# Kernel optimization log

Measured on AMD Instinct MI355X. Metric: run time of the kernel, lower is better.

Reference implementation:

```python
import jax, jax.numpy as jnp
import numpy as np

D_MODEL = 2048
N_HEADS = 16
HEAD_DIM = D_MODEL // N_HEADS  # 128
B, S = 4, 2048


def setup_inputs() -> dict:
    key = jax.random.key(0)
    ks = jax.random.split(key, 7)
    scale = 1.0 / np.sqrt(D_MODEL)
    return {
        "x": jax.random.normal(ks[0], (B, S, D_MODEL), dtype=jnp.float32),
        "cos": jax.random.uniform(ks[1], (S, HEAD_DIM // 2), dtype=jnp.float32),
        "sin": jax.random.uniform(ks[2], (S, HEAD_DIM // 2), dtype=jnp.float32),
        "Wq": jax.random.normal(ks[3], (D_MODEL, D_MODEL), dtype=jnp.float32) * scale,
        "Wk": jax.random.normal(ks[4], (D_MODEL, D_MODEL), dtype=jnp.float32) * scale,
        "Wv": jax.random.normal(ks[5], (D_MODEL, D_MODEL), dtype=jnp.float32) * scale,
        "Wo": jax.random.normal(ks[6], (D_MODEL, D_MODEL), dtype=jnp.float32) * scale,
    }


def apply_rope(x, cos, sin):
    # x: [B, H, S, head_dim]; cos/sin: [S, half] (split-in-half RoPE)
    half = x.shape[-1] // 2
    x1, x2 = x[..., :half], x[..., half:]
    cos = cos[None, None, :, :].astype(x.dtype)
    sin = sin[None, None, :, :].astype(x.dtype)
    return jnp.concatenate([x1 * cos - x2 * sin, x1 * sin + x2 * cos], axis=-1)


def reference(x, cos, sin, Wq, Wk, Wv, Wo):
    Bx, Sx, _ = x.shape
    # nn.Linear: y = x @ W.T
    def proj(W):
        y = jnp.einsum("bsd,ed->bse", x, W)
        return y.reshape(Bx, Sx, N_HEADS, HEAD_DIM).transpose(0, 2, 1, 3)  # [B,H,S,hd]
    q = apply_rope(proj(Wq), cos, sin)
    k = apply_rope(proj(Wk), cos, sin)
    v = proj(Wv)
    scale = 1.0 / np.sqrt(HEAD_DIM)
    scores = jnp.einsum("bhqd,bhkd->bhqk", q, k) * scale  # [B,H,S,S]
    attn = jax.nn.softmax(scores, axis=-1)
    out = jnp.einsum("bhqk,bhkd->bhqd", attn, v)
    out = out.transpose(0, 2, 1, 3).reshape(Bx, Sx, D_MODEL)
    return jnp.einsum("bsd,ed->bse", out, Wo)
```

## Files before the change

### kernel.cpp

```cpp
#include <hip/hip_runtime.h>

typedef _Float16 half_t;
typedef __attribute__((ext_vector_type(8))) _Float16 half8;
typedef __attribute__((ext_vector_type(4))) _Float16 half4v;
typedef __attribute__((ext_vector_type(4))) float f32x4;

#define MFMA16(a,b,c) __builtin_amdgcn_mfma_f32_16x16x32_f16((a),(b),(c),0,0,0)

__device__ __forceinline__ void gld_lds16(const half_t* g, half_t* l){
    __builtin_amdgcn_global_load_lds((__attribute__((address_space(1))) void*)(g),
                                     (__attribute__((address_space(3))) void*)(l), 16, 0, 0);
}

__global__ __launch_bounds__(256) void cvt_k(const float* __restrict__ s, half_t* __restrict__ d, int n4){
    int i = blockIdx.x * 256 + threadIdx.x;
    if (i < n4){
        float4 v = ((const float4*)s)[i];
        half4v h = { (half_t)v.x, (half_t)v.y, (half_t)v.z, (half_t)v.w };
        ((half4v*)d)[i] = h;
    }
}

__global__ __launch_bounds__(256) void cvtw_k(const float* __restrict__ w0, const float* __restrict__ w1,
                                              const float* __restrict__ w2, const float* __restrict__ w3,
                                              half_t* __restrict__ dst){
    const float* srcs[4] = {w0, w1, w2, w3};
    const float* s = srcs[blockIdx.y];
    int i = blockIdx.x * 256 + threadIdx.x;
    float4 v = ((const float4*)s)[i];
    half4v h = { (half_t)v.x, (half_t)v.y, (half_t)v.z, (half_t)v.w };
    ((half4v*)(dst))[(size_t)blockIdx.y * 1048576 + i] = h;
}

__global__ __launch_bounds__(256) void gemm_nt(const half_t* __restrict__ A, const half_t* __restrict__ B,
                                               half_t* __restrict__ Qw, half_t* __restrict__ Kw,
                                               half_t* __restrict__ Vt, float* __restrict__ Co, int kind){
    const int tid  = threadIdx.x;
    const int lane = tid & 63;
    const int w    = lane >> 4;
    const int l15  = lane & 15;
    const int l7   = lane & 7;
    const int wav  = tid >> 6;
    const int wm   = (wav >> 1) * 64;
    const int wn   = (wav & 1) * 64;
    const int bm   = blockIdx.x;
    const int bn   = blockIdx.y;
    const int KD   = 2048;

    __shared__ __align__(16) half_t smem[16384];
    half_t* As = smem;
    half_t* Bs = smem + 8192;

    f32x4 acc[4][4] = {};

    const half_t* Ab = A + (size_t)bm * 128 * KD;
    const half_t* Bb = B + (size_t)bn * 128 * KD;

    for (int k0 = 0; k0 < KD; k0 += 64){
#pragma unroll
        for (int i = 0; i < 4; i++){
            int c = tid + i*256;
            int r = c >> 3, p = c & 7;
            gld_lds16(Ab + (size_t)r*KD + k0 + ((p ^ (r&7)) << 3), As + c*8);
        }
#pragma unroll
        for (int i = 0; i < 4; i++){
            int c = tid + i*256;
            int r = c >> 3, p = c & 7;
            gld_lds16(Bb + (size_t)r*KD + k0 + ((p ^ (r&7)) << 3), Bs + c*8);
        }
        __syncthreads();
#pragma unroll
        for (int ks = 0; ks < 2; ks++){
            half8 af[4], bf[4];
#pragma unroll
            for (int mi = 0; mi < 4; mi++)
                af[mi] = *(const half8*)(As + (wm + mi*16 + l15)*64 + (((ks*4 + w) ^ l7) << 3));
#pragma unroll
            for (int ni = 0; ni < 4; ni++)
                bf[ni] = *(const half8*)(Bs + (wn + ni*16 + l15)*64 + (((ks*4 + w) ^ l7) << 3));
#pragma unroll
            for (int mi = 0; mi < 4; mi++)
#pragma unroll
                for (int ni = 0; ni < 4; ni++)
                    acc[mi][ni] = MFMA16(af[mi], bf[ni], acc[mi][ni]);
        }
        __syncthreads();
    }

    const int rbase = wm + w*4;
    const int cbase = wn + l15;

    if (kind == 0){
        const int which = bn >> 4;
        const int nb = (bn & 15) * 128;
        if (which < 2){
            half_t* dst = which ? Kw : Qw;
#pragma unroll
            for (int mi = 0; mi < 4; mi++)
#pragma unroll
                for (int ni = 0; ni < 4; ni++)
#pragma unroll
                    for (int r = 0; r < 4; r++){
                        int m = bm*128 + rbase + mi*16 + r;
                        int n = nb + cbase + ni*16;
                        dst[(((size_t)(m>>11)*16 + (n>>7))*2048 + (m&2047))*128 + (n&127)] = (half_t)acc[mi][ni][r];
                    }
        } else {
#pragma unroll
            for (int mi = 0; mi < 4; mi++)
#pragma unroll
                for (int ni = 0; ni < 4; ni++){
                    int m0 = bm*128 + rbase + mi*16;
                    int n  = nb + cbase + ni*16;
                    half4v h = {(half_t)acc[mi][ni][0], (half_t)acc[mi][ni][1],
                                (half_t)acc[mi][ni][2], (half_t)acc[mi][ni][3]};
                    *(half4v*)(Vt + (((size_t)(m0>>11)*16 + (n>>7))*128 + (n&127))*2048 + (m0&2047)) = h;
                }
        }
    } else {
#pragma unroll
        for (int mi = 0; mi < 4; mi++)
#pragma unroll
            for (int ni = 0; ni < 4; ni++)
#pragma unroll
                for (int r = 0; r < 4; r++){
                    int m = bm*128 + rbase + mi*16 + r;
                    int n = bn*128 + cbase + ni*16;
                    Co[(size_t)m*2048 + n] = acc[mi][ni][r];
                }
    }
}

__global__ __launch_bounds__(256) void rope_k(half_t* __restrict__ Qw, half_t* __restrict__ Kw,
                                              const float* __restrict__ cs, const float* __restrict__ sn){
    int t  = blockIdx.x * 256 + threadIdx.x;
    int d  = t & 63;
    int s  = (t >> 6) & 2047;
    int bh = t >> 17;
    float c  = cs[s*64 + d];
    float si = sn[s*64 + d];
    size_t base = ((size_t)bh*2048 + s)*128 + d;
    float q1 = (float)Qw[base], q2 = (float)Qw[base+64];
    Qw[base]    = (half_t)(q1*c - q2*si);
    Qw[base+64] = (half_t)(q1*si + q2*c);
    float k1 = (float)Kw[base], k2 = (float)Kw[base+64];
    Kw[base]    = (half_t)(k1*c - k2*si);
    Kw[base+64] = (half_t)(k1*si + k2*c);
}

__global__ __launch_bounds__(256, 3) void attn_k(const half_t* __restrict__ Q, const half_t* __restrict__ K,
                                                 const half_t* __restrict__ Vt, half_t* __restrict__ AO){
    const int tid  = threadIdx.x;
    const int lane = tid & 63;
    const int w    = lane >> 4;
    const int l15  = lane & 15;
    const int l7   = lane & 7;
    const int wav  = tid >> 6;
    const int qt   = blockIdx.x;
    const int bh   = blockIdx.y;

    __shared__ __align__(16) half_t smem[8192 + 8192 + 4*2304];
    half_t* Ks = smem;
    half_t* Vs = smem + 8192;
    half_t* Ps = smem + 16384 + wav*2304;
    half_t* Ob = smem + wav*4096;

    const half_t* Qb = Q + ((size_t)bh*2048 + qt*128 + wav*32)*128;
    half8 aq[2][4];
#pragma unroll
    for (int qi = 0; qi < 2; qi++)
#pragma unroll
        for (int ks = 0; ks < 4; ks++)
            aq[qi][ks] = *(const half8*)(Qb + (qi*16 + l15)*128 + ks*32 + w*8);

    f32x4 oacc[8][2] = {};
    float m_[2] = {-1e30f, -1e30f};
    float l_[2] = {0.0f, 0.0f};

    const float SSC = 0.08838834764831845f * 1.4426950408889634f;

    for (int kt = 0; kt < 32; kt++){
        const half_t* Kb = K  + ((size_t)bh*2048 + kt*64)*128;
        const half_t* Vb = Vt + (size_t)bh*128*2048 + kt*64;
        __syncthreads();
#pragma unroll
        for (int i = 0; i < 4; i++){
            int c = tid + i*256;
            int key = c >> 4, pc = c & 15;
            gld_lds16(Kb + key*128 + ((pc ^ (key&7)) << 3), Ks + c*8);
        }
#pragma unroll
        for (int i = 0; i < 4; i++){
            int c = tid + i*256;
            int d = c >> 3, pc = c & 7;
            gld_lds16(Vb + (size_t)d*2048 + ((pc ^ (d&7)) << 3), Vs + c*8);
        }
        __syncthreads();

        f32x4 sacc[4][2] = {};
#pragma unroll
        for (int ks = 0; ks < 4; ks++){
#pragma unroll
            for (int t = 0; t < 4; t++){
                half8 kf = *(const half8*)(Ks + (t*16 + l15)*128 + (((ks*4 + w) ^ l7) << 3));
                sacc[t][0] = MFMA16(kf, aq[0][ks], sacc[t][0]);
                sacc[t][1] = MFMA16(kf, aq[1][ks], sacc[t][1]);
            }
        }

#pragma unroll
        for (int qi = 0; qi < 2; qi++){
            float mx = sacc[0][qi][0];
#pragma unroll
            for (int t = 0; t < 4; t++)
#pragma unroll
                for (int r = 0; r < 4; r++) mx = fmaxf(mx, sacc[t][qi][r]);
            mx = fmaxf(mx, __shfl_xor(mx, 16));
            mx = fmaxf(mx, __shfl_xor(mx, 32));
            float mn = fmaxf(m_[qi], mx*SSC);
            float alpha = exp2f(m_[qi] - mn);
            m_[qi] = mn;
            float sum = 0.0f;
#pragma unroll
            for (int t = 0; t < 4; t++){
                float p0 = exp2f(sacc[t][qi][0]*SSC - mn);
                float p1 = exp2f(sacc[t][qi][1]*SSC - mn);
                float p2 = exp2f(sacc[t][qi][2]*SSC - mn);
                float p3 = exp2f(sacc[t][qi][3]*SSC - mn);
                sum += (p0 + p1) + (p2 + p3);
                half4v hv = {(half_t)p0, (half_t)p1, (half_t)p2, (half_t)p3};
                *(half4v*)(Ps + (qi*16 + l15)*72 + t*16 + w*4) = hv;
            }
            sum += __shfl_xor(sum, 16);
            sum += __shfl_xor(sum, 32);
            l_[qi] = l_[qi]*alpha + sum;
#pragma unroll
            for (int t = 0; t < 8; t++)
#pragma unroll
                for (int r = 0; r < 4; r++) oacc[t][qi][r] *= alpha;
        }

#pragma unroll
        for (int c2 = 0; c2 < 2; c2++){
            half8 pf0 = *(const half8*)(Ps + l15*72        + c2*32 + w*8);
            half8 pf1 = *(const half8*)(Ps + (16 + l15)*72 + c2*32 + w*8);
#pragma unroll
            for (int t = 0; t < 8; t++){
                half8 vf = *(const half8*)(Vs + (t*16 + l15)*64 + (((c2*4 + w) ^ l7) << 3));
                oacc[t][0] = MFMA16(vf, pf0, oacc[t][0]);
                oacc[t][1] = MFMA16(vf, pf1, oacc[t][1]);
            }
        }
    }

    float inv[2] = {1.0f / l_[0], 1.0f / l_[1]};
    __syncthreads();
#pragma unroll
    for (int t = 0; t < 8; t++)
#pragma unroll
        for (int qi = 0; qi < 2; qi++){
            int q  = qi*16 + l15;
            int c8 = t*2 + (w>>1);
            int pc = c8 ^ l7;
            half4v hv = {(half_t)(oacc[t][qi][0]*inv[qi]), (half_t)(oacc[t][qi][1]*inv[qi]),
                         (half_t)(oacc[t][qi][2]*inv[qi]), (half_t)(oacc[t][qi][3]*inv[qi])};
            *(half4v*)(Ob + q*128 + pc*8 + (w&1)*4) = hv;
        }
    const int b = bh >> 4, h = bh & 15;
#pragma unroll
    for (int it = 0; it < 8; it++){
        int q  = it*4 + w;
        half8 rd = *(const half8*)(Ob + q*128 + ((l15 ^ (q&7)) << 3));
        int s = qt*128 + wav*32 + q;
        *(half8*)(AO + ((size_t)(b*2048 + s))*2048 + h*128 + l15*8) = rd;
    }
}

extern "C" void kernel_launch(void* const* d_in, const int* in_sizes, int n_in,
                              void* d_out, int out_size, void* d_ws, size_t ws_size,
                              hipStream_t stream){
    const float* x  = (const float*)d_in[0];
    const float* cs = (const float*)d_in[1];
    const float* sn = (const float*)d_in[2];
    const float* Wq = (const float*)d_in[3];
    const float* Wk = (const float*)d_in[4];
    const float* Wv = (const float*)d_in[5];
    const float* Wo = (const float*)d_in[6];

    half_t* ws = (half_t*)d_ws;
    half_t* xh = ws;
    half_t* w4 = ws + (size_t)16777216;
    half_t* qw = ws + (size_t)33554432;
    half_t* kw = ws + (size_t)50331648;
    half_t* vt = ws + (size_t)67108864;
    half_t* ao = ws + (size_t)83886080;

    cvt_k<<<16384, 256, 0, stream>>>(x, xh, 4194304);
    cvtw_k<<<dim3(4096, 4), 256, 0, stream>>>(Wq, Wk, Wv, Wo, w4);

    gemm_nt<<<dim3(64, 48), 256, 0, stream>>>(xh, w4, qw, kw, vt, nullptr, 0);
    rope_k<<<32768, 256, 0, stream>>>(qw, kw, cs, sn);
    attn_k<<<dim3(16, 64), 256, 0, stream>>>(qw, kw, vt, ao);
    gemm_nt<<<dim3(64, 16), 256, 0, stream>>>(ao, w4 + 12582912, nullptr, nullptr, nullptr,
                                              (float*)d_out, 1);
}
```

Measured before the change: 786.7 us.

## Replace GEMM with 256x256 multi-stage pipelined kernel and skip redundant softmax rescale

The 128x128 single-buffered GEMM becomes a 512-thread, 256x256-tile kernel. It uses a multi-stage LDS pipeline with direct global-to-LDS loads, explicit vmcnt waits, barriers, MFMA priority boosts and a swizzled workgroup order for L2 reuse. The goal is to hide load latency and raise MFMA utilisation in the QKV and output projections. Separately, the attention softmax now skips the alpha rescale of the accumulators when no lane's running max increases. Risks are fewer workgroups per CU from the 128KB LDS footprint and fragile hand-scheduled wait counts.

```diff
diff --git a/kernel.cpp b/kernel.cpp
--- a/kernel.cpp
+++ b/kernel.cpp
@@ -32,103 +32,121 @@
     ((half4v*)(dst))[(size_t)blockIdx.y * 1048576 + i] = h;
 }
 
-__global__ __launch_bounds__(256) void gemm_nt(const half_t* __restrict__ A, const half_t* __restrict__ B,
-                                               half_t* __restrict__ Qw, half_t* __restrict__ Kw,
-                                               half_t* __restrict__ Vt, float* __restrict__ Co, int kind){
+#define VMWAIT_(n) asm volatile("s_waitcnt vmcnt(" #n ")" ::: "memory")
+#define VMWAIT(n)  VMWAIT_(n)
+
+#define STAGE8(hh) { \
+    const int Tt2 = (hh) >> 2, jj2 = (hh) & 3; \
+    half_t* db = smem + ((jj2 & 1) << 15) + ((Tt2 & 1) << 14) + ((jj2 >> 1) << 13); \
+    const half_t* Gs = ((jj2 & 1) ? Bg : Ag) + Tt2*64 + ((jj2 >> 1) << 5); \
+    gld_lds16(Gs + off0, db + d0); \
+    gld_lds16(Gs + off1, db + d1); \
+}
+
+#define PHASE8(Tt, jj, hh, VMN) { \
+    half_t* Ah = smem + (((Tt) & 1) << 14) + (((jj) >> 1) << 13); \
+    half_t* Bh = Ah + 32768; \
+    half8 af[4], bf[4]; \
+    _Pragma("unroll") for (int x = 0; x < 4; x++) af[x] = *(const half8*)(Ah + (((jj)&1)*4 + x)*1024 + cA); \
+    _Pragma("unroll") for (int y = 0; y < 4; y++) bf[y] = *(const half8*)(Bh + y*1024 + cB); \
+    if ((hh) < 128) STAGE8(hh); \
+    if ((jj) & 1) VMWAIT(VMN); \
+    asm volatile("s_barrier" ::: "memory"); \
+    __builtin_amdgcn_s_setprio(1); \
+    _Pragma("unroll") for (int x = 0; x < 4; x++) \
+      _Pragma("unroll") for (int y = 0; y < 4; y++) \
+        acc[((jj)&1)*4 + x][y] = MFMA16(af[x], bf[y], acc[((jj)&1)*4 + x][y]); \
+    __builtin_amdgcn_s_setprio(0); \
+    __builtin_amdgcn_sched_barrier(0); \
+    asm volatile("s_barrier" ::: "memory"); \
+}
+
+__global__ __launch_bounds__(512) void gemm8(const half_t* __restrict__ A, const half_t* __restrict__ B,
+                                             half_t* __restrict__ Qw, half_t* __restrict__ Kw,
+                                             half_t* __restrict__ Vt, float* __restrict__ Co, int kind){
     const int tid  = threadIdx.x;
     const int lane = tid & 63;
-    const int w    = lane >> 4;
+    const int w4   = lane >> 4;
     const int l15  = lane & 15;
     const int l7   = lane & 7;
     const int wav  = tid >> 6;
-    const int wm   = (wav >> 1) * 64;
-    const int wn   = (wav & 1) * 64;
-    const int bm   = blockIdx.x;
-    const int bn   = blockIdx.y;
-    const int KD   = 2048;
-
-    __shared__ __align__(16) half_t smem[16384];
-    half_t* As = smem;
-    half_t* Bs = smem + 8192;
-
-    f32x4 acc[4][4] = {};
-
-    const half_t* Ab = A + (size_t)bm * 128 * KD;
-    const half_t* Bb = B + (size_t)bn * 128 * KD;
-
-    for (int k0 = 0; k0 < KD; k0 += 64){
-#pragma unroll
-        for (int i = 0; i < 4; i++){
-            int c = tid + i*256;
-            int r = c >> 3, p = c & 7;
-            gld_lds16(Ab + (size_t)r*KD + k0 + ((p ^ (r&7)) << 3), As + c*8);
-        }
-#pragma unroll
-        for (int i = 0; i < 4; i++){
-            int c = tid + i*256;
-            int r = c >> 3, p = c & 7;
-            gld_lds16(Bb + (size_t)r*KD + k0 + ((p ^ (r&7)) << 3), Bs + c*8);
-        }
-        __syncthreads();
-#pragma unroll
-        for (int ks = 0; ks < 2; ks++){
-            half8 af[4], bf[4];
-#pragma unroll
-            for (int mi = 0; mi < 4; mi++)
-                af[mi] = *(const half8*)(As + (wm + mi*16 + l15)*64 + (((ks*4 + w) ^ l7) << 3));
-#pragma unroll
-            for (int ni = 0; ni < 4; ni++)
-                bf[ni] = *(const half8*)(Bs + (wn + ni*16 + l15)*64 + (((ks*4 + w) ^ l7) << 3));
-#pragma unroll
-            for (int mi = 0; mi < 4; mi++)
-#pragma unroll
-                for (int ni = 0; ni < 4; ni++)
-                    acc[mi][ni] = MFMA16(af[mi], bf[ni], acc[mi][ni]);
-        }
-        __syncthreads();
-    }
-
-    const int rbase = wm + w*4;
-    const int cbase = wn + l15;
+    const int wavM = wav >> 2;
+    const int wnq  = wav & 3;
+
+    const int nwg = gridDim.x;
+    const int wg  = blockIdx.x;
+    const int swz = (wg & 7) * (nwg >> 3) + (wg >> 3);
+    const int bm  = swz & 31;
+    const int bn  = swz >> 5;
+
+    __shared__ __align__(16) half_t smem[65536];
+
+    const half_t* Ag = A + (size_t)bm * 256 * 2048;
+    const half_t* Bg = B + (size_t)bn * 256 * 2048;
+
+    const int p0  = tid >> 3, q0 = tid & 7, c0 = q0 ^ (p0 & 7);
+    const int off0 = (p0 + ((c0 >> 2) << 7)) * 2048 + ((c0 & 3) << 3);
+    const int off1 = off0 + 131072;
+    const int d0  = tid * 8, d1 = d0 + 4096;
+
+    const int cA = l15*64 + (((w4 | (wavM << 2)) ^ l7) << 3);
+    const int cB = ((wnq & 1)*64 + l15)*64 + (((w4 | ((wnq >> 1) << 2)) ^ l7) << 3);
+
+    f32x4 acc[8][4] = {};
+
+#pragma unroll
+    for (int h = 0; h < 6; h++) STAGE8(h);
+    VMWAIT(4);
+    asm volatile("s_barrier" ::: "memory");
+
+    for (int it = 0; it < 15; it++){
+        const int h0 = it*8 + 6;
+        PHASE8(2*it,   0, h0,     6); PHASE8(2*it,   1, h0 + 1, 6);
+        PHASE8(2*it,   2, h0 + 2, 6); PHASE8(2*it,   3, h0 + 3, 6);
+        PHASE8(2*it+1, 0, h0 + 4, 6); PHASE8(2*it+1, 1, h0 + 5, 6);
+        PHASE8(2*it+1, 2, h0 + 6, 6); PHASE8(2*it+1, 3, h0 + 7, 6);
+    }
+    PHASE8(30, 0, 126, 6); PHASE8(30, 1, 127, 6);
+    PHASE8(30, 2, 128, 6); PHASE8(30, 3, 129, 2);
+    PHASE8(31, 0, 130, 0); PHASE8(31, 1, 131, 0);
+    PHASE8(31, 2, 132, 0); PHASE8(31, 3, 133, 0);
+
+    const int mB = bm*256 + wavM*128 + w4*4;
+    const int nB = bn*256 + wnq*64 + l15;
 
     if (kind == 0){
-        const int which = bn >> 4;
-        const int nb = (bn & 15) * 128;
-        if (which < 2){
-            half_t* dst = which ? Kw : Qw;
-#pragma unroll
-            for (int mi = 0; mi < 4; mi++)
-#pragma unroll
-                for (int ni = 0; ni < 4; ni++)
+#pragma unroll
+        for (int mi = 0; mi < 8; mi++)
+#pragma unroll
+            for (int ni = 0; ni < 4; ni++){
+                int n  = nB + ni*16;
+                int which = n >> 11;
+                int nb = n & 2047;
+                int m0 = mB + mi*16;
+                if (which < 2){
+                    half_t* dst = which ? Kw : Qw;
 #pragma unroll
                     for (int r = 0; r < 4; r++){
-                        int m = bm*128 + rbase + mi*16 + r;
-                        int n = nb + cbase + ni*16;
-                        dst[(((size_t)(m>>11)*16 + (n>>7))*2048 + (m&2047))*128 + (n&127)] = (half_t)acc[mi][ni][r];
+                        int m = m0 + r;
+                        dst[(((size_t)(m >> 11)*16 + (nb >> 7))*2048 + (m & 2047))*128 + (nb & 127)] = (half_t)acc[mi][ni][r];
                     }
-        } else {
-#pragma unroll
-            for (int mi = 0; mi < 4; mi++)
-#pragma unroll
-                for (int ni = 0; ni < 4; ni++){
-                    int m0 = bm*128 + rbase + mi*16;
-                    int n  = nb + cbase + ni*16;
-                    half4v h = {(half_t)acc[mi][ni][0], (half_t)acc[mi][ni][1],
-                                (half_t)acc[mi][ni][2], (half_t)acc[mi][ni][3]};
-                    *(half4v*)(Vt + (((size_t)(m0>>11)*16 + (n>>7))*128 + (n&127))*2048 + (m0&2047)) = h;
+                } else {
+                    half4v hv = {(half_t)acc[mi][ni][0], (half_t)acc[mi][ni][1],
+                                 (half_t)acc[mi][ni][2], (half_t)acc[mi][ni][3]};
+                    *(half4v*)(Vt + (((size_t)(m0 >> 11)*16 + (nb >> 7))*128 + (nb & 127))*2048 + (m0 & 2047)) = hv;
                 }
-        }
+            }
     } else {
 #pragma unroll
-        for (int mi = 0; mi < 4; mi++)
-#pragma unroll
-            for (int ni = 0; ni < 4; ni++)
-#pragma unroll
-                for (int r = 0; r < 4; r++){
-                    int m = bm*128 + rbase + mi*16 + r;
-                    int n = bn*128 + cbase + ni*16;
-                    Co[(size_t)m*2048 + n] = acc[mi][ni][r];
-                }
+        for (int mi = 0; mi < 8; mi++)
+#pragma unroll
+            for (int ni = 0; ni < 4; ni++){
+                int n  = nB + ni*16;
+                int m0 = mB + mi*16;
+#pragma unroll
+                for (int r = 0; r < 4; r++)
+                    Co[(size_t)(m0 + r)*2048 + n] = acc[mi][ni][r];
+            }
     }
 }
 
@@ -218,27 +236,33 @@
                 for (int r = 0; r < 4; r++) mx = fmaxf(mx, sacc[t][qi][r]);
             mx = fmaxf(mx, __shfl_xor(mx, 16));
             mx = fmaxf(mx, __shfl_xor(mx, 32));
-            float mn = fmaxf(m_[qi], mx*SSC);
-            float alpha = exp2f(m_[qi] - mn);
-            m_[qi] = mn;
+            float mxs = mx * SSC;
+            unsigned long long upd = __ballot(mxs > m_[qi]);
+            if (upd){
+                float mn    = fmaxf(m_[qi], mxs);
+                float alpha = exp2f(m_[qi] - mn);
+                m_[qi] = mn;
+                l_[qi] *= alpha;
+#pragma unroll
+                for (int t = 0; t < 8; t++)
+#pragma unroll
+                    for (int r = 0; r < 4; r++) oacc[t][qi][r] *= alpha;
+            }
+            float mq = m_[qi];
             float sum = 0.0f;
 #pragma unroll
             for (int t = 0; t < 4; t++){
-                float p0 = exp2f(sacc[t][qi][0]*SSC - mn);
-                float p1 = exp2f(sacc[t][qi][1]*SSC - mn);
-                float p2 = exp2f(sacc[t][qi][2]*SSC - mn);
-                float p3 = exp2f(sacc[t][qi][3]*SSC - mn);
+                float p0 = exp2f(sacc[t][qi][0]*SSC - mq);
+                float p1 = exp2f(sacc[t][qi][1]*SSC - mq);
+                float p2 = exp2f(sacc[t][qi][2]*SSC - mq);
+                float p3 = exp2f(sacc[t][qi][3]*SSC - mq);
                 sum += (p0 + p1) + (p2 + p3);
                 half4v hv = {(half_t)p0, (half_t)p1, (half_t)p2, (half_t)p3};
                 *(half4v*)(Ps + (qi*16 + l15)*72 + t*16 + w*4) = hv;
             }
             sum += __shfl_xor(sum, 16);
             sum += __shfl_xor(sum, 32);
-            l_[qi] = l_[qi]*alpha + sum;
-#pragma unroll
-            for (int t = 0; t < 8; t++)
-#pragma unroll
-                for (int r = 0; r < 4; r++) oacc[t][qi][r] *= alpha;
+            l_[qi] += sum;
         }
 
 #pragma unroll
@@ -299,9 +323,9 @@
     cvt_k<<<16384, 256, 0, stream>>>(x, xh, 4194304);
     cvtw_k<<<dim3(4096, 4), 256, 0, stream>>>(Wq, Wk, Wv, Wo, w4);
 
-    gemm_nt<<<dim3(64, 48), 256, 0, stream>>>(xh, w4, qw, kw, vt, nullptr, 0);
+    gemm8<<<768, 512, 0, stream>>>(xh, w4, qw, kw, vt, nullptr, 0);
     rope_k<<<32768, 256, 0, stream>>>(qw, kw, cs, sn);
     attn_k<<<dim3(16, 64), 256, 0, stream>>>(qw, kw, vt, ao);
-    gemm_nt<<<dim3(64, 16), 256, 0, stream>>>(ao, w4 + 12582912, nullptr, nullptr, nullptr,
-                                              (float*)d_out, 1);
-}
+    gemm8<<<256, 512, 0, stream>>>(ao, w4 + 12582912, nullptr, nullptr, nullptr,
+                                   (float*)d_out, 1);
+}
```

New measurement: 733.4 us. -6.8%, faster.
